# Kernel optimization log

Measured on AMD Instinct MI355X. Metric: run time of the kernel, lower is better.

## Reference

```python
import jax, jax.numpy as jnp
import numpy as np

B, N, D = 64, 256, 768
ITER_STEPS = 1


def _linear_w(key, out_d, in_d):
    s = 1.0 / np.sqrt(in_d)
    return jax.random.uniform(key, (out_d, in_d), jnp.float32, -s, s)


def setup_inputs() -> dict:
    key = jax.random.key(0)
    ks = jax.random.split(key, 16)
    node = jax.random.normal(ks[0], (B, N, D), jnp.float32)
    node_mask = jnp.ones((B, N), jnp.int32)
    argument_graph = jax.random.randint(ks[1], (B, N, N), 0, 2, jnp.int32)
    punctuation_graph = jax.random.randint(ks[2], (B, N, N), 0, 2, jnp.int32)
    inp = {
        "node": node,
        "node_mask": node_mask,
        "argument_graph": argument_graph,
        "punctuation_graph": punctuation_graph,
        # node-relatedness scorer: Linear(D, 1, bias=True)
        "Wq": _linear_w(ks[3], 1, D),
        "bq": jnp.zeros((1,), jnp.float32),
        # self node fc: Linear(D, D, bias=True)
        "Ws": _linear_w(ks[4], D, D),
        "bs": jnp.zeros((D,), jnp.float32),
        # 8 relation projections, Linear(D, D, bias=False)
        "Wa": _linear_w(ks[5], D, D),
        "Wp": _linear_w(ks[6], D, D),
        "Wap": _linear_w(ks[7], D, D),
        "Wpp": _linear_w(ks[8], D, D),
        "Wa2": _linear_w(ks[9], D, D),
        "Wp2": _linear_w(ks[10], D, D),
        "Wap2": _linear_w(ks[11], D, D),
        "Wpp2": _linear_w(ks[12], D, D),
    }
    return inp


def reference(node, node_mask, argument_graph, punctuation_graph,
              Wq, bq, Ws, bs, Wa, Wp, Wap, Wpp, Wa2, Wp2, Wap2, Wpp2):
    f32 = jnp.float32
    mask = node_mask.astype(f32)                      # [B, N]
    n = node.shape[1]
    eye = jnp.eye(n, dtype=f32)
    # dd_graph: node_mask outer product with zeroed diagonal
    dd = mask[:, None, :] * mask[:, :, None] * (1.0 - eye)   # [B, N, N]
    g_a = dd * argument_graph.astype(f32)
    g_p = dd * punctuation_graph.astype(f32)
    # reverse directed edges
    g_ar = dd * jnp.swapaxes(g_a, 1, 2)
    g_pr = dd * jnp.swapaxes(g_p, 1, 2)
    neigh = g_a.sum(-1) + g_p.sum(-1) + g_ar.sum(-1) + g_pr.sum(-1)  # [B, N]
    denom = jnp.where(neigh >= 1.0, neigh, 1.0)

    all_weight = []
    for _ in range(ITER_STEPS):
        # (1) node relatedness
        dw = jax.nn.sigmoid(jnp.einsum('bnd,od->bno', node, Wq) + bq)[..., 0]  # [B, N]
        all_weight.append(dw)
        self_info = jnp.einsum('bnd,ed->bne', node, Ws) + bs

        def msg(g, W):
            # node_weight: broadcast dw over rows, zero where no edge
            nw = dw[:, None, :] * g                    # [B, N, N]
            proj = jnp.einsum('bnd,ed->bne', node, W)  # [B, N, D]
            return jnp.matmul(nw, proj)                # [B, N, D]

        agg = (msg(g_a, Wa) + msg(g_p, Wp) + msg(g_ar, Wap) + msg(g_pr, Wpp)
               + msg(g_a, Wa2) + msg(g_p, Wp2) + msg(g_ar, Wap2) + msg(g_pr, Wpp2))
        agg = agg / denom[..., None]
        # (3) node update
        node = jax.nn.relu(self_info + agg)

    all_weight = jnp.stack(all_weight, axis=1)  # [B, steps, N]
    return node, all_weight
```

## Files before the change

kernel.cpp:

```cpp
#include <hip/hip_runtime.h>
#include <hip/hip_bf16.h>
#include <math.h>

typedef __bf16 bf16;
typedef __bf16 bf16x8 __attribute__((ext_vector_type(8)));
typedef __bf16 bf16x4 __attribute__((ext_vector_type(4)));
typedef float f32x4 __attribute__((ext_vector_type(4)));

#define BB 64
#define NN 256
#define DD 768
#define MM (BB*NN)
#define KP 1024
#define WSZ (DD*DD)
#define TLD 136

__device__ __forceinline__ void async16(const void* g, void* l) {
  __builtin_amdgcn_global_load_lds((__attribute__((address_space(1))) void*)g,
                                   (__attribute__((address_space(3))) void*)l,
                                   16, 0, 0);
}

__device__ __forceinline__ void stage_tile(const bf16* gsrc, int ld, char* ldst,
                                           int wv, int lane) {
#pragma unroll
  for (int cc = 0; cc < 2; ++cc) {
    int c = wv * 2 + cc;
    int row = c * 16 + (lane >> 2);
    int col = (lane & 3) * 8;
    async16(gsrc + (size_t)row * ld + col, ldst + c * 1024);
  }
}

__device__ __forceinline__ void mma_step(const char* lA, const char* lB,
                                         f32x4 acc[4][4], int lane, int wr, int wc) {
  bf16x8 af[4], bfr[4];
  int rbase = wr * 64 + (lane & 15);
  int cbase = wc * 64 + (lane & 15);
  int ko = (lane >> 4) * 8;
#pragma unroll
  for (int r = 0; r < 4; ++r)
    af[r] = *(const bf16x8*)(lA + (((rbase + r * 16) * 32) + ko) * 2);
#pragma unroll
  for (int c = 0; c < 4; ++c)
    bfr[c] = *(const bf16x8*)(lB + (((cbase + c * 16) * 32) + ko) * 2);
#pragma unroll
  for (int r = 0; r < 4; ++r)
#pragma unroll
    for (int c = 0; c < 4; ++c)
      acc[r][c] = __builtin_amdgcn_mfma_f32_16x16x32_bf16(af[r], bfr[c], acc[r][c], 0, 0, 0);
}

__device__ __forceinline__ void k_step64(const bf16* Ab, int lda, const bf16* Bb, int ldb,
                                         char* smem, f32x4 acc[4][4],
                                         int wv, int lane, int wr, int wc) {
  char* lA0 = smem;
  char* lA1 = smem + 8192;
  char* lB0 = smem + 16384;
  char* lB1 = smem + 24576;
  __syncthreads();
  stage_tile(Ab, lda, lA0, wv, lane);
  stage_tile(Ab + 32, lda, lA1, wv, lane);
  stage_tile(Bb, ldb, lB0, wv, lane);
  stage_tile(Bb + 32, ldb, lB1, wv, lane);
  __builtin_amdgcn_s_waitcnt(0);
  __syncthreads();
  mma_step(lA0, lB0, acc, lane, wr, wc);
  mma_step(lA1, lB1, acc, lane, wr, wc);
}

__global__ void k_pre(const float* __restrict__ node, const float* __restrict__ Wq,
                      const float* __restrict__ bq, bf16* __restrict__ node_bf,
                      float* __restrict__ dw, float* __restrict__ allw,
                      float* __restrict__ neigh,
                      const float* __restrict__ Ws,
                      const float* __restrict__ Wa, const float* __restrict__ Wp,
                      const float* __restrict__ Wap, const float* __restrict__ Wpp,
                      const float* __restrict__ Wa2, const float* __restrict__ Wp2,
                      const float* __restrict__ Wap2, const float* __restrict__ Wpp2,
                      bf16* __restrict__ Wcat4, bf16* __restrict__ Ws_bf) {
  if (blockIdx.x < MM / 4) {
    int lane = threadIdx.x & 63, wv = threadIdx.x >> 6;
    int row = blockIdx.x * 4 + wv;
    const float* nr = node + (size_t)row * DD;
    bf16* nb = node_bf + (size_t)row * DD;
    float s = 0.f;
#pragma unroll
    for (int k = 0; k < DD / 64; ++k) {
      int idx = lane + k * 64;
      float v = nr[idx];
      nb[idx] = (bf16)v;
      s += v * Wq[idx];
    }
#pragma unroll
    for (int off = 32; off; off >>= 1) s += __shfl_down(s, off);
    if (lane == 0) {
      float z = s + bq[0];
      float d = 1.f / (1.f + expf(-z));
      dw[row] = d;
      allw[row] = d;
      neigh[row] = 0.f;
    }
  } else {
    int i = (blockIdx.x - MM / 4) * 256 + threadIdx.x;
    Ws_bf[i] = (bf16)Ws[i];
    Wcat4[i]           = (bf16)(Wa[i] + Wa2[i]);
    Wcat4[i + WSZ]     = (bf16)(Wp[i] + Wp2[i]);
    Wcat4[i + 2 * WSZ] = (bf16)(Wap[i] + Wap2[i]);
    Wcat4[i + 3 * WSZ] = (bf16)(Wpp[i] + Wpp2[i]);
  }
}

__global__ void k_graph(const int* __restrict__ mask, const int* __restrict__ arg,
                        const int* __restrict__ pun, const float* __restrict__ dw,
                        bf16* __restrict__ g_bf, float* __restrict__ neigh) {
  __shared__ float la[64][65];
  __shared__ float lp[64][65];
  __shared__ float msk[256];
  __shared__ float dwv[256];
  int tid = threadIdx.x;
  int bi = blockIdx.x;
  int b = bi >> 4, it = (bi >> 2) & 3, jt = bi & 3;
  int i0 = it * 64, j0 = jt * 64;
  msk[tid] = (float)mask[b * NN + tid];
  dwv[tid] = dw[b * NN + tid];
  __syncthreads();
  int ir = tid >> 2, c4 = (tid & 3) * 16;
  int i = i0 + ir;
  float mi = msk[i];
  size_t gb = (size_t)b * NN * NN;
  const int* ap = arg + gb + (size_t)i * NN + j0 + c4;
  const int* pp = pun + gb + (size_t)i * NN + j0 + c4;
  union { bf16 h[16]; bf16x8 v[2]; } oa, op;
  float racc = 0.f;
#pragma unroll
  for (int k = 0; k < 16; ++k) {
    int j = j0 + c4 + k;
    float dd = (i == j) ? 0.f : mi * msk[j];
    float ga = dd * (float)ap[k];
    float gp = dd * (float)pp[k];
    la[ir][c4 + k] = ga;
    lp[ir][c4 + k] = gp;
    float w = dwv[j];
    oa.h[k] = (bf16)(w * ga);
    op.h[k] = (bf16)(w * gp);
    racc += ga + gp;
  }
  bf16* d0p = g_bf + ((size_t)(b * NN + i) * 4 + 0) * NN + j0 + c4;
  bf16* d1p = g_bf + ((size_t)(b * NN + i) * 4 + 1) * NN + j0 + c4;
  *(bf16x8*)d0p = oa.v[0]; *(bf16x8*)(d0p + 8) = oa.v[1];
  *(bf16x8*)d1p = op.v[0]; *(bf16x8*)(d1p + 8) = op.v[1];
  racc += __shfl_xor(racc, 1);
  racc += __shfl_xor(racc, 2);
  if ((tid & 3) == 0) atomicAdd(&neigh[b * NN + i], racc);
  __syncthreads();
  int jr = ir, ic4 = c4;
  float cacc = 0.f;
#pragma unroll
  for (int k = 0; k < 16; ++k) {
    float ga = la[ic4 + k][jr];
    float gp = lp[ic4 + k][jr];
    float w = dwv[i0 + ic4 + k];
    oa.h[k] = (bf16)(w * ga);
    op.h[k] = (bf16)(w * gp);
    cacc += ga + gp;
  }
  bf16* d2p = g_bf + ((size_t)(b * NN + j0 + jr) * 4 + 2) * NN + i0 + ic4;
  bf16* d3p = g_bf + ((size_t)(b * NN + j0 + jr) * 4 + 3) * NN + i0 + ic4;
  *(bf16x8*)d2p = oa.v[0]; *(bf16x8*)(d2p + 8) = oa.v[1];
  *(bf16x8*)d3p = op.v[0]; *(bf16x8*)(d3p + 8) = op.v[1];
  cacc += __shfl_xor(cacc, 1);
  cacc += __shfl_xor(cacc, 2);
  if ((tid & 3) == 0) atomicAdd(&neigh[b * NN + j0 + jr], cacc);
}

__global__ __launch_bounds__(256) void k_proj(const bf16* __restrict__ node_bf,
                                              const bf16* __restrict__ Wcat4,
                                              bf16* __restrict__ projT) {
  __shared__ __align__(16) char smem[32768];
  int tid = threadIdx.x, lane = tid & 63, wv = tid >> 6, wr = wv >> 1, wc = wv & 1;
  int m0 = blockIdx.x * 128;
  int n0 = blockIdx.y * 128;
  const bf16* Ab = node_bf + (size_t)m0 * DD;
  const bf16* Bb = Wcat4 + (size_t)n0 * DD;
  f32x4 z = {0.f, 0.f, 0.f, 0.f};
  f32x4 acc[4][4];
#pragma unroll
  for (int r = 0; r < 4; ++r)
#pragma unroll
    for (int c = 0; c < 4; ++c) acc[r][c] = z;
  for (int k0 = 0; k0 < DD; k0 += 64)
    k_step64(Ab + k0, DD, Bb + k0, DD, smem, acc, wv, lane, wr, wc);
  __syncthreads();
  int b = m0 >> 8, j0 = m0 & 255;
  int X = n0 / DD, e0 = n0 - X * DD;
  bf16* tb = (bf16*)smem;
  bf16* obase = projT + ((size_t)b * DD + e0) * KP + X * NN + j0;
#pragma unroll
  for (int p = 0; p < 2; ++p) {
    if (wc == p) {
#pragma unroll
      for (int r = 0; r < 4; ++r)
#pragma unroll
        for (int c = 0; c < 4; ++c) {
          int nn = c * 16 + (lane & 15);
          int mm = wr * 64 + r * 16 + ((lane >> 4) << 2);
          bf16x4 o;
#pragma unroll
          for (int q = 0; q < 4; ++q) o[q] = (bf16)acc[r][c][q];
          *(bf16x4*)(tb + nn * TLD + mm) = o;
        }
    }
    __syncthreads();
#pragma unroll
    for (int t = 0; t < 4; ++t) {
      int row = t * 16 + (tid >> 4);
      int cc8 = (tid & 15) * 8;
      bf16x8 v = *(const bf16x8*)(tb + row * TLD + cc8);
      *(bf16x8*)(obase + ((size_t)(p * 64 + row)) * KP + cc8) = v;
    }
    __syncthreads();
  }
}

__global__ __launch_bounds__(256) void k_agg(const bf16* __restrict__ g_bf,
                                             const bf16* __restrict__ projT,
                                             const bf16* __restrict__ node_bf,
                                             const bf16* __restrict__ Ws_bf,
                                             const float* __restrict__ neigh,
                                             const float* __restrict__ bs,
                                             float* __restrict__ out) {
  __shared__ __align__(16) char smem[32768];
  int tid = threadIdx.x, lane = tid & 63, wv = tid >> 6, wr = wv >> 1, wc = wv & 1;
  int b = blockIdx.y;
  int it = blockIdx.x / 6, et = blockIdx.x % 6;
  int i0 = it * 128, e0 = et * 128;
  f32x4 z = {0.f, 0.f, 0.f, 0.f};
  f32x4 acc[4][4];
#pragma unroll
  for (int r = 0; r < 4; ++r)
#pragma unroll
    for (int c = 0; c < 4; ++c) acc[r][c] = z;
  const bf16* Ab = g_bf + (size_t)(b * NN + i0) * KP;
  const bf16* Bb = projT + ((size_t)b * DD + e0) * KP;
  for (int k0 = 0; k0 < KP; k0 += 64)
    k_step64(Ab + k0, KP, Bb + k0, KP, smem, acc, wv, lane, wr, wc);
  int rowb = i0 + wr * 64 + (lane >> 4) * 4;
#pragma unroll
  for (int r = 0; r < 4; ++r)
#pragma unroll
    for (int q = 0; q < 4; ++q) {
      float rd = 1.f / fmaxf(neigh[b * NN + rowb + r * 16 + q], 1.f);
#pragma unroll
      for (int c = 0; c < 4; ++c) acc[r][c][q] *= rd;
    }
  const bf16* Ab2 = node_bf + (size_t)(b * NN + i0) * DD;
  const bf16* Bb2 = Ws_bf + (size_t)e0 * DD;
  for (int k0 = 0; k0 < DD; k0 += 64)
    k_step64(Ab2 + k0, DD, Bb2 + k0, DD, smem, acc, wv, lane, wr, wc);
  int colb = e0 + wc * 64 + (lane & 15);
#pragma unroll
  for (int c = 0; c < 4; ++c) {
    int col = colb + c * 16;
    float bv = bs[col];
#pragma unroll
    for (int r = 0; r < 4; ++r)
#pragma unroll
      for (int q = 0; q < 4; ++q) {
        int m = b * NN + rowb + r * 16 + q;
        out[(size_t)m * DD + col] = fmaxf(acc[r][c][q] + bv, 0.f);
      }
  }
}

extern "C" void kernel_launch(void* const* d_in, const int* in_sizes, int n_in,
                              void* d_out, int out_size, void* d_ws, size_t ws_size,
                              hipStream_t stream) {
  const float* node = (const float*)d_in[0];
  const int* mask   = (const int*)d_in[1];
  const int* arg    = (const int*)d_in[2];
  const int* pun    = (const int*)d_in[3];
  const float* Wq   = (const float*)d_in[4];
  const float* bq   = (const float*)d_in[5];
  const float* Ws   = (const float*)d_in[6];
  const float* bs   = (const float*)d_in[7];
  const float* Wa   = (const float*)d_in[8];
  const float* Wp   = (const float*)d_in[9];
  const float* Wap  = (const float*)d_in[10];
  const float* Wpp  = (const float*)d_in[11];
  const float* Wa2  = (const float*)d_in[12];
  const float* Wp2  = (const float*)d_in[13];
  const float* Wap2 = (const float*)d_in[14];
  const float* Wpp2 = (const float*)d_in[15];

  float* out  = (float*)d_out;
  float* allw = out + (size_t)MM * DD;

  char* ws = (char*)d_ws;
  bf16* node_bf = (bf16*)ws;
  float* dw     = (float*)(ws + 25165824);
  float* neigh  = (float*)(ws + 25231360);
  bf16* Wcat4   = (bf16*)(ws + 25296896);
  bf16* Ws_bf   = (bf16*)(ws + 30015488);
  bf16* g_bf    = (bf16*)(ws + 31195136);
  bf16* projT   = (bf16*)(ws + 64749568);
  (void)ws_size; (void)in_sizes; (void)n_in; (void)out_size;

  k_pre<<<MM / 4 + WSZ / 256, 256, 0, stream>>>(node, Wq, bq, node_bf, dw, allw, neigh,
                                                Ws, Wa, Wp, Wap, Wpp,
                                                Wa2, Wp2, Wap2, Wpp2, Wcat4, Ws_bf);
  k_graph<<<BB * 16, 256, 0, stream>>>(mask, arg, pun, dw, g_bf, neigh);
  k_proj<<<dim3(128, 24), 256, 0, stream>>>(node_bf, Wcat4, projT);
  k_agg<<<dim3(12, BB), 256, 0, stream>>>(g_bf, projT, node_bf, Ws_bf, neigh, bs, out);
}
```

Before: 362.2 us.

## Store graph weights and projections in fp8 and aggregate with fp8 MFMA

The weighted graph matrices and the projected node features are now written as fp8 instead of bf16. The aggregation GEMM stages 128-wide K chunks and uses fp8 MFMA instructions, which halves the intermediate memory traffic and the LDS footprint per K step. The aggregation grid is also flattened and remapped so that blocks sharing a batch land on the same XCD, aiming at better L2 reuse. The cost is lower precision in the message-passing sum, since fp8 projections carry only a few mantissa bits, which risks tolerance failures.

New measurement: 330.6 us. 1.1x faster.

```diff
diff --git a/kernel.cpp b/kernel.cpp
--- a/kernel.cpp
+++ b/kernel.cpp
@@ -3,8 +3,8 @@
 #include <math.h>
 
 typedef __bf16 bf16;
+typedef unsigned char u8;
 typedef __bf16 bf16x8 __attribute__((ext_vector_type(8)));
-typedef __bf16 bf16x4 __attribute__((ext_vector_type(4)));
 typedef float f32x4 __attribute__((ext_vector_type(4)));
 
 #define BB 64
@@ -13,7 +13,7 @@
 #define MM (BB*NN)
 #define KP 1024
 #define WSZ (DD*DD)
-#define TLD 136
+#define TL 144
 
 __device__ __forceinline__ void async16(const void* g, void* l) {
   __builtin_amdgcn_global_load_lds((__attribute__((address_space(1))) void*)g,
@@ -30,6 +30,13 @@
     int col = (lane & 3) * 8;
     async16(gsrc + (size_t)row * ld + col, ldst + c * 1024);
   }
+}
+
+__device__ __forceinline__ void stage_fp8(const u8* gsrc, int ld, char* ldst,
+                                          int wv, int lane) {
+  int row = wv * 32 + (lane >> 1);
+  int col = (lane & 1) * 16;
+  async16(gsrc + (size_t)row * ld + col, ldst + wv * 1024);
 }
 
 __device__ __forceinline__ void mma_step(const char* lA, const char* lB,
@@ -49,6 +56,25 @@
 #pragma unroll
     for (int c = 0; c < 4; ++c)
       acc[r][c] = __builtin_amdgcn_mfma_f32_16x16x32_bf16(af[r], bfr[c], acc[r][c], 0, 0, 0);
+}
+
+__device__ __forceinline__ void mma_step_fp8(const char* lA, const char* lB,
+                                             f32x4 acc[4][4], int lane, int wr, int wc) {
+  long af[4], bfr[4];
+  int rbase = wr * 64 + (lane & 15);
+  int cbase = wc * 64 + (lane & 15);
+  int ko = (lane >> 4) * 8;
+#pragma unroll
+  for (int r = 0; r < 4; ++r)
+    af[r] = *(const long*)(lA + (rbase + r * 16) * 32 + ko);
+#pragma unroll
+  for (int c = 0; c < 4; ++c)
+    bfr[c] = *(const long*)(lB + (cbase + c * 16) * 32 + ko);
+#pragma unroll
+  for (int r = 0; r < 4; ++r)
+#pragma unroll
+    for (int c = 0; c < 4; ++c)
+      acc[r][c] = __builtin_amdgcn_mfma_f32_16x16x32_fp8_fp8(af[r], bfr[c], acc[r][c], 0, 0, 0);
 }
 
 __device__ __forceinline__ void k_step64(const bf16* Ab, int lda, const bf16* Bb, int ldb,
@@ -67,6 +93,13 @@
   __syncthreads();
   mma_step(lA0, lB0, acc, lane, wr, wc);
   mma_step(lA1, lB1, acc, lane, wr, wc);
+}
+
+__device__ __forceinline__ unsigned pack4(float a, float b, float c, float d) {
+  int w = 0;
+  w = __builtin_amdgcn_cvt_pk_fp8_f32(a, b, w, false);
+  w = __builtin_amdgcn_cvt_pk_fp8_f32(c, d, w, true);
+  return (unsigned)w;
 }
 
 __global__ void k_pre(const float* __restrict__ node, const float* __restrict__ Wq,
@@ -113,7 +146,7 @@
 
 __global__ void k_graph(const int* __restrict__ mask, const int* __restrict__ arg,
                         const int* __restrict__ pun, const float* __restrict__ dw,
-                        bf16* __restrict__ g_bf, float* __restrict__ neigh) {
+                        u8* __restrict__ g8, float* __restrict__ neigh) {
   __shared__ float la[64][65];
   __shared__ float lp[64][65];
   __shared__ float msk[256];
@@ -131,7 +164,7 @@
   size_t gb = (size_t)b * NN * NN;
   const int* ap = arg + gb + (size_t)i * NN + j0 + c4;
   const int* pp = pun + gb + (size_t)i * NN + j0 + c4;
-  union { bf16 h[16]; bf16x8 v[2]; } oa, op;
+  float va[16], vp[16];
   float racc = 0.f;
 #pragma unroll
   for (int k = 0; k < 16; ++k) {
@@ -142,14 +175,18 @@
     la[ir][c4 + k] = ga;
     lp[ir][c4 + k] = gp;
     float w = dwv[j];
-    oa.h[k] = (bf16)(w * ga);
-    op.h[k] = (bf16)(w * gp);
+    va[k] = w * ga;
+    vp[k] = w * gp;
     racc += ga + gp;
   }
-  bf16* d0p = g_bf + ((size_t)(b * NN + i) * 4 + 0) * NN + j0 + c4;
-  bf16* d1p = g_bf + ((size_t)(b * NN + i) * 4 + 1) * NN + j0 + c4;
-  *(bf16x8*)d0p = oa.v[0]; *(bf16x8*)(d0p + 8) = oa.v[1];
-  *(bf16x8*)d1p = op.v[0]; *(bf16x8*)(d1p + 8) = op.v[1];
+  uint4 oa, op;
+#pragma unroll
+  for (int g = 0; g < 4; ++g) {
+    (&oa.x)[g] = pack4(va[g*4], va[g*4+1], va[g*4+2], va[g*4+3]);
+    (&op.x)[g] = pack4(vp[g*4], vp[g*4+1], vp[g*4+2], vp[g*4+3]);
+  }
+  *(uint4*)(g8 + (size_t)(b * NN + i) * KP + 0 * NN + j0 + c4) = oa;
+  *(uint4*)(g8 + (size_t)(b * NN + i) * KP + 1 * NN + j0 + c4) = op;
   racc += __shfl_xor(racc, 1);
   racc += __shfl_xor(racc, 2);
   if ((tid & 3) == 0) atomicAdd(&neigh[b * NN + i], racc);
@@ -161,14 +198,17 @@
     float ga = la[ic4 + k][jr];
     float gp = lp[ic4 + k][jr];
     float w = dwv[i0 + ic4 + k];
-    oa.h[k] = (bf16)(w * ga);
-    op.h[k] = (bf16)(w * gp);
+    va[k] = w * ga;
+    vp[k] = w * gp;
     cacc += ga + gp;
   }
-  bf16* d2p = g_bf + ((size_t)(b * NN + j0 + jr) * 4 + 2) * NN + i0 + ic4;
-  bf16* d3p = g_bf + ((size_t)(b * NN + j0 + jr) * 4 + 3) * NN + i0 + ic4;
-  *(bf16x8*)d2p = oa.v[0]; *(bf16x8*)(d2p + 8) = oa.v[1];
-  *(bf16x8*)d3p = op.v[0]; *(bf16x8*)(d3p + 8) = op.v[1];
+#pragma unroll
+  for (int g = 0; g < 4; ++g) {
+    (&oa.x)[g] = pack4(va[g*4], va[g*4+1], va[g*4+2], va[g*4+3]);
+    (&op.x)[g] = pack4(vp[g*4], vp[g*4+1], vp[g*4+2], vp[g*4+3]);
+  }
+  *(uint4*)(g8 + (size_t)(b * NN + j0 + jr) * KP + 2 * NN + i0 + ic4) = oa;
+  *(uint4*)(g8 + (size_t)(b * NN + j0 + jr) * KP + 3 * NN + i0 + ic4) = op;
   cacc += __shfl_xor(cacc, 1);
   cacc += __shfl_xor(cacc, 2);
   if ((tid & 3) == 0) atomicAdd(&neigh[b * NN + j0 + jr], cacc);
@@ -176,7 +216,7 @@
 
 __global__ __launch_bounds__(256) void k_proj(const bf16* __restrict__ node_bf,
                                               const bf16* __restrict__ Wcat4,
-                                              bf16* __restrict__ projT) {
+                                              u8* __restrict__ p8) {
   __shared__ __align__(16) char smem[32768];
   int tid = threadIdx.x, lane = tid & 63, wv = tid >> 6, wr = wv >> 1, wc = wv & 1;
   int m0 = blockIdx.x * 128;
@@ -194,37 +234,29 @@
   __syncthreads();
   int b = m0 >> 8, j0 = m0 & 255;
   int X = n0 / DD, e0 = n0 - X * DD;
-  bf16* tb = (bf16*)smem;
-  bf16* obase = projT + ((size_t)b * DD + e0) * KP + X * NN + j0;
-#pragma unroll
-  for (int p = 0; p < 2; ++p) {
-    if (wc == p) {
-#pragma unroll
-      for (int r = 0; r < 4; ++r)
-#pragma unroll
-        for (int c = 0; c < 4; ++c) {
-          int nn = c * 16 + (lane & 15);
-          int mm = wr * 64 + r * 16 + ((lane >> 4) << 2);
-          bf16x4 o;
-#pragma unroll
-          for (int q = 0; q < 4; ++q) o[q] = (bf16)acc[r][c][q];
-          *(bf16x4*)(tb + nn * TLD + mm) = o;
-        }
-    }
-    __syncthreads();
-#pragma unroll
-    for (int t = 0; t < 4; ++t) {
-      int row = t * 16 + (tid >> 4);
-      int cc8 = (tid & 15) * 8;
-      bf16x8 v = *(const bf16x8*)(tb + row * TLD + cc8);
-      *(bf16x8*)(obase + ((size_t)(p * 64 + row)) * KP + cc8) = v;
-    }
-    __syncthreads();
-  }
-}
-
-__global__ __launch_bounds__(256) void k_agg(const bf16* __restrict__ g_bf,
-                                             const bf16* __restrict__ projT,
+  u8* tb = (u8*)smem;
+#pragma unroll
+  for (int r = 0; r < 4; ++r)
+#pragma unroll
+    for (int c = 0; c < 4; ++c) {
+      int n = wc * 64 + c * 16 + (lane & 15);
+      int m = wr * 64 + r * 16 + ((lane >> 4) << 2);
+      *(unsigned*)(tb + n * TL + m) =
+          pack4(acc[r][c][0], acc[r][c][1], acc[r][c][2], acc[r][c][3]);
+    }
+  __syncthreads();
+  u8* obase = p8 + ((size_t)b * DD + e0) * KP + X * NN + j0;
+#pragma unroll
+  for (int t = 0; t < 4; ++t) {
+    int row = t * 32 + (tid >> 3);
+    int col = (tid & 7) * 16;
+    uint4 v = *(const uint4*)(tb + row * TL + col);
+    *(uint4*)(obase + (size_t)row * KP + col) = v;
+  }
+}
+
+__global__ __launch_bounds__(256) void k_agg(const u8* __restrict__ g8,
+                                             const u8* __restrict__ p8,
                                              const bf16* __restrict__ node_bf,
                                              const bf16* __restrict__ Ws_bf,
                                              const float* __restrict__ neigh,
@@ -232,19 +264,32 @@
                                              float* __restrict__ out) {
   __shared__ __align__(16) char smem[32768];
   int tid = threadIdx.x, lane = tid & 63, wv = tid >> 6, wr = wv >> 1, wc = wv & 1;
-  int b = blockIdx.y;
-  int it = blockIdx.x / 6, et = blockIdx.x % 6;
-  int i0 = it * 128, e0 = et * 128;
+  int l = blockIdx.x;
+  int xcd = l & 7, idx = l >> 3;
+  int b = (idx / 12) * 8 + xcd;
+  int t = idx % 12;
+  int i0 = (t / 6) * 128, e0 = (t % 6) * 128;
   f32x4 z = {0.f, 0.f, 0.f, 0.f};
   f32x4 acc[4][4];
 #pragma unroll
   for (int r = 0; r < 4; ++r)
 #pragma unroll
     for (int c = 0; c < 4; ++c) acc[r][c] = z;
-  const bf16* Ab = g_bf + (size_t)(b * NN + i0) * KP;
-  const bf16* Bb = projT + ((size_t)b * DD + e0) * KP;
-  for (int k0 = 0; k0 < KP; k0 += 64)
-    k_step64(Ab + k0, KP, Bb + k0, KP, smem, acc, wv, lane, wr, wc);
+  const u8* Ab = g8 + (size_t)(b * NN + i0) * KP;
+  const u8* Bb = p8 + ((size_t)b * DD + e0) * KP;
+  for (int k0 = 0; k0 < KP; k0 += 128) {
+    __syncthreads();
+#pragma unroll
+    for (int s = 0; s < 4; ++s) {
+      stage_fp8(Ab + k0 + s * 32, KP, smem + s * 4096, wv, lane);
+      stage_fp8(Bb + k0 + s * 32, KP, smem + 16384 + s * 4096, wv, lane);
+    }
+    __builtin_amdgcn_s_waitcnt(0);
+    __syncthreads();
+#pragma unroll
+    for (int s = 0; s < 4; ++s)
+      mma_step_fp8(smem + s * 4096, smem + 16384 + s * 4096, acc, lane, wr, wc);
+  }
   int rowb = i0 + wr * 64 + (lane >> 4) * 4;
 #pragma unroll
   for (int r = 0; r < 4; ++r)
@@ -302,14 +347,14 @@
   float* neigh  = (float*)(ws + 25231360);
   bf16* Wcat4   = (bf16*)(ws + 25296896);
   bf16* Ws_bf   = (bf16*)(ws + 30015488);
-  bf16* g_bf    = (bf16*)(ws + 31195136);
-  bf16* projT   = (bf16*)(ws + 64749568);
+  u8*   g8      = (u8*)(ws + 31195136);
+  u8*   p8      = (u8*)(ws + 47972352);
   (void)ws_size; (void)in_sizes; (void)n_in; (void)out_size;
 
   k_pre<<<MM / 4 + WSZ / 256, 256, 0, stream>>>(node, Wq, bq, node_bf, dw, allw, neigh,
                                                 Ws, Wa, Wp, Wap, Wpp,
                                                 Wa2, Wp2, Wap2, Wpp2, Wcat4, Ws_bf);
-  k_graph<<<BB * 16, 256, 0, stream>>>(mask, arg, pun, dw, g_bf, neigh);
-  k_proj<<<dim3(128, 24), 256, 0, stream>>>(node_bf, Wcat4, projT);
-  k_agg<<<dim3(12, BB), 256, 0, stream>>>(g_bf, projT, node_bf, Ws_bf, neigh, bs, out);
-}
+  k_graph<<<BB * 16, 256, 0, stream>>>(mask, arg, pun, dw, g8, neigh);
+  k_proj<<<dim3(128, 24), 256, 0, stream>>>(node_bf, Wcat4, p8);
+  k_agg<<<12 * BB, 256, 0, stream>>>(g8, p8, node_bf, Ws_bf, neigh, bs, out);
+}
```
